# Kernel optimization log

Measured on AMD Instinct MI355X. Metric: run time of the kernel, lower is better.

Reference implementation:

```python
import jax, jax.numpy as jnp
import numpy as np

N = 100000      # nodes
E = 1600000     # edges (avg degree 16)
IN_DIM = 256
HID = 128
EPS = 0.3


def setup_inputs() -> dict:
    key = jax.random.key(0)
    ks = jax.random.split(key, 6)
    x = jax.random.normal(ks[0], (N, IN_DIM), dtype=jnp.float32)
    # edges without self-loops (dst = src + nonzero offset mod N)
    src = jax.random.randint(ks[1], (E,), 0, N)
    off = jax.random.randint(ks[2], (E,), 1, N)
    dst = (src + off) % N
    edge_index = jnp.stack([src, dst]).astype(jnp.int32)
    # xavier_normal_ with gain=1.414 for t1 and gate
    g1 = 1.414 * np.sqrt(2.0 / (IN_DIM + HID))
    w1 = (jax.random.normal(ks[3], (HID, IN_DIM)) * g1).astype(jnp.float32)
    b1 = jnp.zeros((HID,), jnp.float32)
    gg = 1.414 * np.sqrt(2.0 / (2 * HID + 1))
    gate_w = (jax.random.normal(ks[4], (1, 2 * HID)) * gg).astype(jnp.float32)
    gate_b = jnp.zeros((1,), jnp.float32)
    return dict(x=x, edge_index=edge_index, w1=w1, b1=b1, gate_w=gate_w, gate_b=gate_b)


def reference(x, edge_index, w1, b1, gate_w, gate_b):
    src, dst = edge_index[0], edge_index[1]
    # in-degree based symmetric norm, deg clamped to >= 1
    deg = jax.ops.segment_sum(jnp.ones((E,), jnp.float32), dst, num_segments=N)
    norm = jnp.clip(deg, 1.0) ** -0.5  # [N]

    h = jax.nn.relu(x @ w1.T + b1)     # [N, HID] (dropout p=0 / eval -> identity)
    raw = h

    # gate([h_dst, h_src]) decomposed: concat @ W^T = h_dst @ w_d + h_src @ w_s
    w_d, w_s = gate_w[0, :HID], gate_w[0, HID:]
    a_dst = h @ w_d                    # [N]
    a_src = h @ w_s                    # [N]
    g = jnp.tanh(a_dst[dst] + a_src[src] + gate_b[0])   # [E] per-edge gate
    e = g * norm[dst] * norm[src]                        # [E]

    # u_mul_e + sum: gather src features, weight, scatter-add to dst
    z = jax.ops.segment_sum(h[src] * e[:, None], dst, num_segments=N)  # [N, HID]
    return EPS * raw + z
```

## Files before the change

kernel.cpp:

```cpp
#include <hip/hip_runtime.h>
#include <math.h>
#include <stdint.h>

#define N_NODES 100000
#define N_EDGES 1600000
#define IN_DIM  256
#define HID     128
#define EPS_C   0.3f

#define NPB      128
#define NBKT     782
#define NBKT_P   784
#define BCAP     3072
#define S1_CHUNK 4096
#define S1_BLOCKS 391

#define PK_SRC(p)  ((p) & 0x1FFFF)
#define PK_LI(p)   ((p) >> 17)

typedef __attribute__((ext_vector_type(8))) __bf16 bf16x8;
typedef __attribute__((ext_vector_type(4))) float  f32x4;
typedef __attribute__((ext_vector_type(8))) unsigned short ushort8;

static __device__ __forceinline__ unsigned short f2bf(float f) {
    unsigned u = __float_as_uint(f);
    unsigned r = (u + 0x7fffu + ((u >> 16) & 1u)) >> 16;
    return (unsigned short)r;
}
static __device__ __forceinline__ float bf2f(unsigned short s) {
    return __uint_as_float((unsigned)s << 16);
}
static __device__ __forceinline__ float fast_tanh(float x) {
    float e = __builtin_exp2f(x * 2.8853900817779268f);
    return 1.0f - 2.0f / (e + 1.0f);
}

__global__ __launch_bounds__(256) void convert_w1_kernel(const float* __restrict__ w1,
                                                         unsigned short* __restrict__ w1b) {
    int i = blockIdx.x * 256 + threadIdx.x;
    if (i * 4 >= HID * IN_DIM) return;
    float4 v = *(const float4*)&w1[i * 4];
    ushort4 r;
    r.x = f2bf(v.x); r.y = f2bf(v.y); r.z = f2bf(v.z); r.w = f2bf(v.w);
    *(ushort4*)&w1b[i * 4] = r;
}

__global__ __launch_bounds__(512) void partition_kernel(const int* __restrict__ src,
                                                        const int* __restrict__ dst,
                                                        int* __restrict__ gcur,
                                                        int* __restrict__ ebuf) {
    __shared__ int hist[NBKT_P];
    __shared__ int base[NBKT_P];
    __shared__ int gpos[NBKT_P];
    __shared__ int cur[NBKT_P];
    __shared__ int seg[512];
    __shared__ int2 staged[S1_CHUNK];

    int t = threadIdx.x;
    for (int i = t; i < NBKT_P; i += 512) hist[i] = 0;
    __syncthreads();

    int base4 = blockIdx.x * (S1_CHUNK / 4);
    int rem4  = N_EDGES / 4 - base4;

    int4 sv[2], dv[2];
#pragma unroll
    for (int j = 0; j < 2; j++) {
        int i4 = j * 512 + t;
        if (i4 < rem4) {
            sv[j] = *(const int4*)&src[(base4 + i4) * 4];
            dv[j] = *(const int4*)&dst[(base4 + i4) * 4];
        } else {
            dv[j] = make_int4(-1, -1, -1, -1);
        }
    }
#pragma unroll
    for (int j = 0; j < 2; j++) {
        if (dv[j].x >= 0) {
            atomicAdd(&hist[dv[j].x >> 7], 1);
            atomicAdd(&hist[dv[j].y >> 7], 1);
            atomicAdd(&hist[dv[j].z >> 7], 1);
            atomicAdd(&hist[dv[j].w >> 7], 1);
        }
    }
    __syncthreads();

    int h0 = 0, h1 = 0;
    if (t < NBKT_P / 2) { h0 = hist[2 * t]; h1 = hist[2 * t + 1]; }
    seg[t] = h0 + h1;
    __syncthreads();
    for (int off = 1; off < 512; off <<= 1) {
        int a = (t >= off) ? seg[t - off] : 0;
        __syncthreads();
        seg[t] += a;
        __syncthreads();
    }
    if (t < NBKT_P / 2) {
        int excl = seg[t] - (h0 + h1);
        base[2 * t]     = excl;
        cur[2 * t]      = excl;
        base[2 * t + 1] = excl + h0;
        cur[2 * t + 1]  = excl + h0;
        if (h0 > 0) gpos[2 * t]     = atomicAdd(&gcur[2 * t], h0);
        if (h1 > 0) gpos[2 * t + 1] = atomicAdd(&gcur[2 * t + 1], h1);
    }
    __syncthreads();

#pragma unroll
    for (int j = 0; j < 2; j++) {
        if (dv[j].x >= 0) {
            int p;
            p = atomicAdd(&cur[dv[j].x >> 7], 1); staged[p] = make_int2(sv[j].x, dv[j].x);
            p = atomicAdd(&cur[dv[j].y >> 7], 1); staged[p] = make_int2(sv[j].y, dv[j].y);
            p = atomicAdd(&cur[dv[j].z >> 7], 1); staged[p] = make_int2(sv[j].z, dv[j].z);
            p = atomicAdd(&cur[dv[j].w >> 7], 1); staged[p] = make_int2(sv[j].w, dv[j].w);
        }
    }
    __syncthreads();

    int n = N_EDGES - base4 * 4;
    if (n > S1_CHUNK) n = S1_CHUNK;
    for (int i = t; i < n; i += 512) {
        int2 e = staged[i];
        int b = e.y >> 7;
        int off2 = gpos[b] + (i - base[b]);
        if (off2 < BCAP) ebuf[(size_t)b * BCAP + off2] = ((e.y & (NPB - 1)) << 17) | e.x;
    }
}

__global__ __launch_bounds__(512) void bscan_kernel(const int* __restrict__ gcur,
                                                    int* __restrict__ bstart) {
    __shared__ int s[512];
    int t = threadIdx.x;
    int a0 = 0, a1 = 0;
    if (t < NBKT_P / 2) {
        a0 = (2 * t     < NBKT) ? gcur[2 * t]     : 0;
        a1 = (2 * t + 1 < NBKT) ? gcur[2 * t + 1] : 0;
    }
    s[t] = a0 + a1;
    __syncthreads();
    for (int off = 1; off < 512; off <<= 1) {
        int a = (t >= off) ? s[t - off] : 0;
        __syncthreads();
        s[t] += a;
        __syncthreads();
    }
    if (t < NBKT_P / 2) {
        int excl = s[t] - (a0 + a1);
        if (2 * t     < NBKT) bstart[2 * t]     = excl;
        if (2 * t + 1 < NBKT) bstart[2 * t + 1] = excl + a0;
    }
}

__global__ __launch_bounds__(512) void deg_kernel(const int* __restrict__ gcur,
                                                  const int* __restrict__ bstart,
                                                  const int* __restrict__ ebuf,
                                                  int* __restrict__ rowstart,
                                                  float* __restrict__ nrm) {
    __shared__ int dcnt[NPB];
    __shared__ int s[NPB];
    int b = blockIdx.x;
    int t = threadIdx.x;
    if (t < NPB) dcnt[t] = 0;
    __syncthreads();

    int ecnt = gcur[b];
    if (ecnt > BCAP) ecnt = BCAP;
    for (int j = t; j < ecnt; j += 512)
        atomicAdd(&dcnt[PK_LI(ebuf[(size_t)b * BCAP + j])], 1);
    __syncthreads();

    int v = 0;
    if (t < NPB) { v = dcnt[t]; s[t] = v; }
    __syncthreads();
    for (int off = 1; off < NPB; off <<= 1) {
        int a = (t < NPB && t >= off) ? s[t - off] : 0;
        __syncthreads();
        if (t < NPB) s[t] += a;
        __syncthreads();
    }

    int nbase = b * NPB;
    int nn = N_NODES - nbase;
    if (nn > NPB) nn = NPB;
    if (t < nn) {
        rowstart[nbase + t] = bstart[b] + s[t] - v;
        nrm[nbase + t] = rsqrtf(fmaxf((float)v, 1.0f));
    }
    if (b == NBKT - 1 && t == 0) rowstart[N_NODES] = N_EDGES;
}

__global__ __launch_bounds__(256) void gemm_kernel(const float* __restrict__ x,
                                                   const unsigned short* __restrict__ w1b,
                                                   const float* __restrict__ b1,
                                                   const float* __restrict__ gw,
                                                   const float* __restrict__ nrm,
                                                   unsigned short* __restrict__ h,
                                                   float2* __restrict__ pd_pack,
                                                   float2* __restrict__ ps_pack) {
    __shared__ unsigned short As[256 * 40];
    __shared__ unsigned short Bs[128 * 40];

    int tid = threadIdx.x;
    int bm = blockIdx.x * 256;

    int wv   = tid >> 6;
    int lane = tid & 63;
    int col  = lane & 15;
    int kq   = lane >> 4;

    f32x4 acc[4][8];
#pragma unroll
    for (int f = 0; f < 4; f++)
#pragma unroll
        for (int nf = 0; nf < 8; nf++) acc[f][nf] = (f32x4){0.f, 0.f, 0.f, 0.f};

    int am = tid >> 2;
    int ak = (tid & 3) * 8;
    int bn = tid >> 1;
    int bk = (tid & 1) * 16;

    for (int k0 = 0; k0 < IN_DIM; k0 += 32) {
        ushort8 av[4];
#pragma unroll
        for (int sub = 0; sub < 4; sub++) {
            int r = am + sub * 64;
            float4 a0 = {0,0,0,0}, a1 = {0,0,0,0};
            if (bm + r < N_NODES) {
                const float* p = &x[(size_t)(bm + r) * IN_DIM + k0 + ak];
                a0 = *(const float4*)p;
                a1 = *(const float4*)(p + 4);
            }
            av[sub][0]=f2bf(a0.x); av[sub][1]=f2bf(a0.y);
            av[sub][2]=f2bf(a0.z); av[sub][3]=f2bf(a0.w);
            av[sub][4]=f2bf(a1.x); av[sub][5]=f2bf(a1.y);
            av[sub][6]=f2bf(a1.z); av[sub][7]=f2bf(a1.w);
        }
        ushort8 bv0 = *(const ushort8*)&w1b[bn * IN_DIM + k0 + bk];
        ushort8 bv1 = *(const ushort8*)&w1b[bn * IN_DIM + k0 + bk + 8];

        __syncthreads();
#pragma unroll
        for (int sub = 0; sub < 4; sub++)
            *(ushort8*)&As[(am + sub * 64) * 40 + ak] = av[sub];
        *(ushort8*)&Bs[bn * 40 + bk] = bv0;
        *(ushort8*)&Bs[bn * 40 + bk + 8] = bv1;
        __syncthreads();

        bf16x8 afrag[4];
#pragma unroll
        for (int f = 0; f < 4; f++)
            afrag[f] = *(bf16x8*)&As[(wv * 64 + f * 16 + col) * 40 + kq * 8];
#pragma unroll
        for (int nf = 0; nf < 8; nf++) {
            bf16x8 bfrag = *(bf16x8*)&Bs[(nf * 16 + col) * 40 + kq * 8];
#pragma unroll
            for (int f = 0; f < 4; f++)
                acc[f][nf] = __builtin_amdgcn_mfma_f32_16x16x32_bf16(afrag[f], bfrag,
                                                                     acc[f][nf], 0, 0, 0);
        }
    }

    float bias[8], wd[8], wsv[8];
#pragma unroll
    for (int nf = 0; nf < 8; nf++) {
        bias[nf] = b1[nf * 16 + col];
        wd[nf]   = gw[nf * 16 + col];
        wsv[nf]  = gw[HID + nf * 16 + col];
    }
#pragma unroll
    for (int f = 0; f < 4; f++) {
#pragma unroll
        for (int r = 0; r < 4; r++) {
            int gm = bm + wv * 64 + f * 16 + kq * 4 + r;
            float pd = 0.f, ps = 0.f;
            bool ok = (gm < N_NODES);
#pragma unroll
            for (int nf = 0; nf < 8; nf++) {
                float v = fmaxf(acc[f][nf][r] + bias[nf], 0.f);
                pd = fmaf(v, wd[nf], pd);
                ps = fmaf(v, wsv[nf], ps);
                if (ok) h[(size_t)gm * HID + nf * 16 + col] = f2bf(v);
            }
#pragma unroll
            for (int m = 1; m < 16; m <<= 1) {
                pd += __shfl_xor(pd, m);
                ps += __shfl_xor(ps, m);
            }
            if (ok && col == 0) {
                float nv = nrm[gm];
                pd_pack[gm] = make_float2(pd, nv);
                ps_pack[gm] = make_float2(ps, nv);
            }
        }
    }
}

__global__ __launch_bounds__(512) void scatter2_kernel(const int* __restrict__ gcur,
                                                       const int* __restrict__ ebuf,
                                                       const int* __restrict__ rowstart,
                                                       const float2* __restrict__ pd_pack,
                                                       const float2* __restrict__ ps_pack,
                                                       const float* __restrict__ gb,
                                                       int2* __restrict__ epack) {
    __shared__ int    curs[NPB];
    __shared__ float2 pdl[NPB];
    int b = blockIdx.x;
    int t = threadIdx.x;
    int nbase = b * NPB;
    int nn = N_NODES - nbase;
    if (nn > NPB) nn = NPB;
    if (t < nn) {
        curs[t] = rowstart[nbase + t];
        pdl[t]  = pd_pack[nbase + t];
    }
    __syncthreads();

    int ecnt = gcur[b];
    if (ecnt > BCAP) ecnt = BCAP;
    float gbv = gb[0];
    for (int j = t; j < ecnt; j += 512) {
        int p = ebuf[(size_t)b * BCAP + j];
        int s  = PK_SRC(p);
        int li = PK_LI(p);
        int pos = atomicAdd(&curs[li], 1);
        float2 pdp = pdl[li];
        float2 psp = ps_pack[s];
        float g = fast_tanh(pdp.x + psp.x + gbv);
        epack[pos] = make_int2(s, __float_as_int(g * pdp.y * psp.y));
    }
}

__global__ __launch_bounds__(256) void aggregate_kernel(const int* __restrict__ rowstart,
                                                        const int2* __restrict__ epack,
                                                        const unsigned short* __restrict__ h,
                                                        float* __restrict__ out) {
    int node = blockIdx.x * 4 + (threadIdx.x >> 6);
    if (node >= N_NODES) return;
    int lane = threadIdx.x & 63;
    int q  = lane >> 4;
    int ql = lane & 15;

    int beg = rowstart[node];
    int end = rowstart[node + 1];

    float acc[8];
#pragma unroll
    for (int t = 0; t < 8; t++) acc[t] = 0.f;

    int j = beg;
    for (; j + 8 <= end; j += 8) {
        int2 e0 = epack[j + q];
        int2 e1 = epack[j + 4 + q];
        ushort8 r0 = *(const ushort8*)&h[(size_t)e0.x * HID + ql * 8];
        ushort8 r1 = *(const ushort8*)&h[(size_t)e1.x * HID + ql * 8];
        float c0 = __int_as_float(e0.y);
        float c1 = __int_as_float(e1.y);
#pragma unroll
        for (int t = 0; t < 8; t++) {
            acc[t] = fmaf(c0, bf2f(r0[t]), acc[t]);
            acc[t] = fmaf(c1, bf2f(r1[t]), acc[t]);
        }
    }
    for (; j < end; j += 4) {
        bool act = (j + q) < end;
        int idx = act ? (j + q) : beg;
        int2 e = epack[idx];
        ushort8 r = *(const ushort8*)&h[(size_t)e.x * HID + ql * 8];
        float c = act ? __int_as_float(e.y) : 0.f;
#pragma unroll
        for (int t = 0; t < 8; t++) acc[t] = fmaf(c, bf2f(r[t]), acc[t]);
    }
#pragma unroll
    for (int t = 0; t < 8; t++) {
        acc[t] += __shfl_xor(acc[t], 16);
        acc[t] += __shfl_xor(acc[t], 32);
    }
    if (q == 0) {
        ushort8 hd = *(const ushort8*)&h[(size_t)node * HID + ql * 8];
        f32x4 o0, o1;
        o0.x = fmaf(EPS_C, bf2f(hd[0]), acc[0]);
        o0.y = fmaf(EPS_C, bf2f(hd[1]), acc[1]);
        o0.z = fmaf(EPS_C, bf2f(hd[2]), acc[2]);
        o0.w = fmaf(EPS_C, bf2f(hd[3]), acc[3]);
        o1.x = fmaf(EPS_C, bf2f(hd[4]), acc[4]);
        o1.y = fmaf(EPS_C, bf2f(hd[5]), acc[5]);
        o1.z = fmaf(EPS_C, bf2f(hd[6]), acc[6]);
        o1.w = fmaf(EPS_C, bf2f(hd[7]), acc[7]);
        __builtin_nontemporal_store(o0, (f32x4*)&out[(size_t)node * HID + ql * 8]);
        __builtin_nontemporal_store(o1, (f32x4*)&out[(size_t)node * HID + ql * 8 + 4]);
    }
}

extern "C" void kernel_launch(void* const* d_in, const int* in_sizes, int n_in,
                              void* d_out, int out_size, void* d_ws, size_t ws_size,
                              hipStream_t stream) {
    const float* x  = (const float*)d_in[0];
    const int*   ei = (const int*)d_in[1];
    const float* w1 = (const float*)d_in[2];
    const float* b1 = (const float*)d_in[3];
    const float* gw = (const float*)d_in[4];
    const float* gb = (const float*)d_in[5];
    float* out = (float*)d_out;

    const int* src = ei;
    const int* dst = ei + N_EDGES;

    uintptr_t base = (uintptr_t)d_ws;
    size_t off = 0;
    auto alloc = [&](size_t bytes) -> void* {
        void* p = (void*)(base + off);
        off += (bytes + 255) & ~(size_t)255;
        return p;
    };
    unsigned short* h   = (unsigned short*)alloc((size_t)N_NODES * HID * 2);
    float2* pd_pack     = (float2*)alloc((size_t)N_NODES * 8);
    float2* ps_pack     = (float2*)alloc((size_t)N_NODES * 8);
    float*  nrm         = (float*)alloc((size_t)N_NODES * 4);
    int*    rowstart    = (int*)alloc((size_t)(N_NODES + 1) * 4);
    int2*   epack       = (int2*)alloc((size_t)N_EDGES * 8);
    unsigned short* w1b = (unsigned short*)alloc((size_t)HID * IN_DIM * 2);
    int*    gcur        = (int*)alloc((size_t)NBKT * 4);
    int*    bstart      = (int*)alloc((size_t)NBKT * 4);
    int*    ebuf        = (int*)alloc((size_t)NBKT * BCAP * 4);

    (void)hipMemsetAsync(gcur, 0, (size_t)NBKT * 4, stream);

    convert_w1_kernel<<<(HID * IN_DIM / 4 + 255) / 256, 256, 0, stream>>>(w1, w1b);
    partition_kernel<<<S1_BLOCKS, 512, 0, stream>>>(src, dst, gcur, ebuf);
    bscan_kernel<<<1, 512, 0, stream>>>(gcur, bstart);
    deg_kernel<<<NBKT, 512, 0, stream>>>(gcur, bstart, ebuf, rowstart, nrm);
    gemm_kernel<<<(N_NODES + 255) / 256, 256, 0, stream>>>(x, w1b, b1, gw, nrm,
                                                           h, pd_pack, ps_pack);
    scatter2_kernel<<<NBKT, 512, 0, stream>>>(gcur, ebuf, rowstart,
                                              pd_pack, ps_pack, gb, epack);
    aggregate_kernel<<<(N_NODES + 3) / 4, 256, 0, stream>>>(rowstart, epack, h, out);
}
```

Baseline: 313.9 us.

## Simplify edge partition, drop bucket scan, restructure GEMM with resident swizzled W

The partition kernel now writes packed edges straight to global buckets from LDS atomic cursors instead of staging and locally scanning them. Bucket counters are padded to 16 ints each to avoid contention on shared cache lines. The global bucket scan kernel is removed: each bucket owns a fixed BCAP-sized region of epack, and per-node (begin, end) pairs are stored as int2. The GEMM is rewritten to keep all of W1 in swizzled LDS, use 128-row tiles with one 16-row MFMA strip per wave, and prefetch A in registers, dropping per-k LDS staging and barriers. The trade-off is scattered global writes in partition and a larger, padded edge buffer.

```diff
diff --git a/kernel.cpp b/kernel.cpp
--- a/kernel.cpp
+++ b/kernel.cpp
@@ -14,6 +14,7 @@
 #define BCAP     3072
 #define S1_CHUNK 4096
 #define S1_BLOCKS 391
+#define GC(b)    ((b) * 16)
 
 #define PK_SRC(p)  ((p) & 0x1FFFF)
 #define PK_LI(p)   ((p) >> 17)
@@ -50,11 +51,7 @@
                                                         int* __restrict__ gcur,
                                                         int* __restrict__ ebuf) {
     __shared__ int hist[NBKT_P];
-    __shared__ int base[NBKT_P];
-    __shared__ int gpos[NBKT_P];
     __shared__ int cur[NBKT_P];
-    __shared__ int seg[512];
-    __shared__ int2 staged[S1_CHUNK];
 
     int t = threadIdx.x;
     for (int i = t; i < NBKT_P; i += 512) hist[i] = 0;
@@ -85,77 +82,32 @@
     }
     __syncthreads();
 
-    int h0 = 0, h1 = 0;
-    if (t < NBKT_P / 2) { h0 = hist[2 * t]; h1 = hist[2 * t + 1]; }
-    seg[t] = h0 + h1;
-    __syncthreads();
-    for (int off = 1; off < 512; off <<= 1) {
-        int a = (t >= off) ? seg[t - off] : 0;
-        __syncthreads();
-        seg[t] += a;
-        __syncthreads();
-    }
     if (t < NBKT_P / 2) {
-        int excl = seg[t] - (h0 + h1);
-        base[2 * t]     = excl;
-        cur[2 * t]      = excl;
-        base[2 * t + 1] = excl + h0;
-        cur[2 * t + 1]  = excl + h0;
-        if (h0 > 0) gpos[2 * t]     = atomicAdd(&gcur[2 * t], h0);
-        if (h1 > 0) gpos[2 * t + 1] = atomicAdd(&gcur[2 * t + 1], h1);
+        int h0 = hist[2 * t], h1 = hist[2 * t + 1];
+        if (h0 > 0) cur[2 * t]     = atomicAdd(&gcur[GC(2 * t)], h0);
+        if (h1 > 0) cur[2 * t + 1] = atomicAdd(&gcur[GC(2 * t + 1)], h1);
     }
     __syncthreads();
 
 #pragma unroll
     for (int j = 0; j < 2; j++) {
         if (dv[j].x >= 0) {
-            int p;
-            p = atomicAdd(&cur[dv[j].x >> 7], 1); staged[p] = make_int2(sv[j].x, dv[j].x);
-            p = atomicAdd(&cur[dv[j].y >> 7], 1); staged[p] = make_int2(sv[j].y, dv[j].y);
-            p = atomicAdd(&cur[dv[j].z >> 7], 1); staged[p] = make_int2(sv[j].z, dv[j].z);
-            p = atomicAdd(&cur[dv[j].w >> 7], 1); staged[p] = make_int2(sv[j].w, dv[j].w);
-        }
-    }
-    __syncthreads();
-
-    int n = N_EDGES - base4 * 4;
-    if (n > S1_CHUNK) n = S1_CHUNK;
-    for (int i = t; i < n; i += 512) {
-        int2 e = staged[i];
-        int b = e.y >> 7;
-        int off2 = gpos[b] + (i - base[b]);
-        if (off2 < BCAP) ebuf[(size_t)b * BCAP + off2] = ((e.y & (NPB - 1)) << 17) | e.x;
-    }
-}
-
-__global__ __launch_bounds__(512) void bscan_kernel(const int* __restrict__ gcur,
-                                                    int* __restrict__ bstart) {
-    __shared__ int s[512];
-    int t = threadIdx.x;
-    int a0 = 0, a1 = 0;
-    if (t < NBKT_P / 2) {
-        a0 = (2 * t     < NBKT) ? gcur[2 * t]     : 0;
-        a1 = (2 * t + 1 < NBKT) ? gcur[2 * t + 1] : 0;
-    }
-    s[t] = a0 + a1;
-    __syncthreads();
-    for (int off = 1; off < 512; off <<= 1) {
-        int a = (t >= off) ? s[t - off] : 0;
-        __syncthreads();
-        s[t] += a;
-        __syncthreads();
-    }
-    if (t < NBKT_P / 2) {
-        int excl = s[t] - (a0 + a1);
-        if (2 * t     < NBKT) bstart[2 * t]     = excl;
-        if (2 * t + 1 < NBKT) bstart[2 * t + 1] = excl + a0;
+            int b, p;
+            b = dv[j].x >> 7; p = atomicAdd(&cur[b], 1);
+            if (p < BCAP) ebuf[(size_t)b * BCAP + p] = ((dv[j].x & (NPB - 1)) << 17) | sv[j].x;
+            b = dv[j].y >> 7; p = atomicAdd(&cur[b], 1);
+            if (p < BCAP) ebuf[(size_t)b * BCAP + p] = ((dv[j].y & (NPB - 1)) << 17) | sv[j].y;
+            b = dv[j].z >> 7; p = atomicAdd(&cur[b], 1);
+            if (p < BCAP) ebuf[(size_t)b * BCAP + p] = ((dv[j].z & (NPB - 1)) << 17) | sv[j].z;
+            b = dv[j].w >> 7; p = atomicAdd(&cur[b], 1);
+            if (p < BCAP) ebuf[(size_t)b * BCAP + p] = ((dv[j].w & (NPB - 1)) << 17) | sv[j].w;
+        }
     }
 }
 
 __global__ __launch_bounds__(512) void deg_kernel(const int* __restrict__ gcur,
-                                                  const int* __restrict__ bstart,
                                                   const int* __restrict__ ebuf,
-                                                  int* __restrict__ rowstart,
+                                                  int2* __restrict__ rs2,
                                                   float* __restrict__ nrm) {
     __shared__ int dcnt[NPB];
     __shared__ int s[NPB];
@@ -164,7 +116,7 @@
     if (t < NPB) dcnt[t] = 0;
     __syncthreads();
 
-    int ecnt = gcur[b];
+    int ecnt = gcur[GC(b)];
     if (ecnt > BCAP) ecnt = BCAP;
     for (int j = t; j < ecnt; j += 512)
         atomicAdd(&dcnt[PK_LI(ebuf[(size_t)b * BCAP + j])], 1);
@@ -184,13 +136,13 @@
     int nn = N_NODES - nbase;
     if (nn > NPB) nn = NPB;
     if (t < nn) {
-        rowstart[nbase + t] = bstart[b] + s[t] - v;
+        int incl = s[t];
+        rs2[nbase + t] = make_int2(b * BCAP + incl - v, b * BCAP + incl);
         nrm[nbase + t] = rsqrtf(fmaxf((float)v, 1.0f));
     }
-    if (b == NBKT - 1 && t == 0) rowstart[N_NODES] = N_EDGES;
-}
-
-__global__ __launch_bounds__(256) void gemm_kernel(const float* __restrict__ x,
+}
+
+__global__ __launch_bounds__(512) void gemm_kernel(const float* __restrict__ x,
                                                    const unsigned short* __restrict__ w1b,
                                                    const float* __restrict__ b1,
                                                    const float* __restrict__ gw,
@@ -198,67 +150,58 @@
                                                    unsigned short* __restrict__ h,
                                                    float2* __restrict__ pd_pack,
                                                    float2* __restrict__ ps_pack) {
-    __shared__ unsigned short As[256 * 40];
-    __shared__ unsigned short Bs[128 * 40];
-
-    int tid = threadIdx.x;
-    int bm = blockIdx.x * 256;
-
+    __shared__ unsigned short Bs[HID * IN_DIM];
+
+    int tid  = threadIdx.x;
+    int bm   = blockIdx.x * 128;
     int wv   = tid >> 6;
     int lane = tid & 63;
     int col  = lane & 15;
     int kq   = lane >> 4;
 
-    f32x4 acc[4][8];
-#pragma unroll
-    for (int f = 0; f < 4; f++)
-#pragma unroll
-        for (int nf = 0; nf < 8; nf++) acc[f][nf] = (f32x4){0.f, 0.f, 0.f, 0.f};
-
-    int am = tid >> 2;
-    int ak = (tid & 3) * 8;
-    int bn = tid >> 1;
-    int bk = (tid & 1) * 16;
+    {
+        int n   = tid >> 2;
+        int k8b = (tid & 3) * 8;
+        const ushort8* srcp = (const ushort8*)&w1b[n * IN_DIM + k8b * 8];
+#pragma unroll
+        for (int j = 0; j < 8; j++) {
+            int k8 = k8b + j;
+            *(ushort8*)((char*)Bs + n * 512 + ((k8 ^ (n & 7)) * 16)) = srcp[j];
+        }
+    }
+
+    f32x4 acc[8];
+#pragma unroll
+    for (int nf = 0; nf < 8; nf++) acc[nf] = (f32x4){0.f, 0.f, 0.f, 0.f};
+
+    int row  = bm + wv * 16 + col;
+    bool rok = row < N_NODES;
+    const float* ap = &x[(size_t)row * IN_DIM + kq * 8];
+
+    float4 a0 = {0, 0, 0, 0}, a1 = {0, 0, 0, 0};
+    if (rok) { a0 = *(const float4*)ap; a1 = *(const float4*)(ap + 4); }
+
+    __syncthreads();
 
     for (int k0 = 0; k0 < IN_DIM; k0 += 32) {
-        ushort8 av[4];
-#pragma unroll
-        for (int sub = 0; sub < 4; sub++) {
-            int r = am + sub * 64;
-            float4 a0 = {0,0,0,0}, a1 = {0,0,0,0};
-            if (bm + r < N_NODES) {
-                const float* p = &x[(size_t)(bm + r) * IN_DIM + k0 + ak];
-                a0 = *(const float4*)p;
-                a1 = *(const float4*)(p + 4);
-            }
-            av[sub][0]=f2bf(a0.x); av[sub][1]=f2bf(a0.y);
-            av[sub][2]=f2bf(a0.z); av[sub][3]=f2bf(a0.w);
-            av[sub][4]=f2bf(a1.x); av[sub][5]=f2bf(a1.y);
-            av[sub][6]=f2bf(a1.z); av[sub][7]=f2bf(a1.w);
-        }
-        ushort8 bv0 = *(const ushort8*)&w1b[bn * IN_DIM + k0 + bk];
-        ushort8 bv1 = *(const ushort8*)&w1b[bn * IN_DIM + k0 + bk + 8];
-
-        __syncthreads();
-#pragma unroll
-        for (int sub = 0; sub < 4; sub++)
-            *(ushort8*)&As[(am + sub * 64) * 40 + ak] = av[sub];
-        *(ushort8*)&Bs[bn * 40 + bk] = bv0;
-        *(ushort8*)&Bs[bn * 40 + bk + 8] = bv1;
-        __syncthreads();
-
-        bf16x8 afrag[4];
-#pragma unroll
-        for (int f = 0; f < 4; f++)
-            afrag[f] = *(bf16x8*)&As[(wv * 64 + f * 16 + col) * 40 + kq * 8];
+        float4 n0 = {0, 0, 0, 0}, n1 = {0, 0, 0, 0};
+        if (k0 + 32 < IN_DIM && rok) {
+            n0 = *(const float4*)(ap + k0 + 32);
+            n1 = *(const float4*)(ap + k0 + 36);
+        }
+        ushort8 av;
+        av[0] = f2bf(a0.x); av[1] = f2bf(a0.y); av[2] = f2bf(a0.z); av[3] = f2bf(a0.w);
+        av[4] = f2bf(a1.x); av[5] = f2bf(a1.y); av[6] = f2bf(a1.z); av[7] = f2bf(a1.w);
+        bf16x8 afrag = *(bf16x8*)&av;
+
+        int swz = ((k0 >> 3) + kq) ^ (col & 7);
 #pragma unroll
         for (int nf = 0; nf < 8; nf++) {
-            bf16x8 bfrag = *(bf16x8*)&Bs[(nf * 16 + col) * 40 + kq * 8];
-#pragma unroll
-            for (int f = 0; f < 4; f++)
-                acc[f][nf] = __builtin_amdgcn_mfma_f32_16x16x32_bf16(afrag[f], bfrag,
-                                                                     acc[f][nf], 0, 0, 0);
-        }
+            int n = nf * 16 + col;
+            bf16x8 bfrag = *(bf16x8*)((char*)Bs + n * 512 + swz * 16);
+            acc[nf] = __builtin_amdgcn_mfma_f32_16x16x32_bf16(afrag, bfrag, acc[nf], 0, 0, 0);
+        }
+        a0 = n0; a1 = n1;
     }
 
     float bias[8], wd[8], wsv[8];
@@ -269,36 +212,33 @@
         wsv[nf]  = gw[HID + nf * 16 + col];
     }
 #pragma unroll
-    for (int f = 0; f < 4; f++) {
-#pragma unroll
-        for (int r = 0; r < 4; r++) {
-            int gm = bm + wv * 64 + f * 16 + kq * 4 + r;
-            float pd = 0.f, ps = 0.f;
-            bool ok = (gm < N_NODES);
-#pragma unroll
-            for (int nf = 0; nf < 8; nf++) {
-                float v = fmaxf(acc[f][nf][r] + bias[nf], 0.f);
-                pd = fmaf(v, wd[nf], pd);
-                ps = fmaf(v, wsv[nf], ps);
-                if (ok) h[(size_t)gm * HID + nf * 16 + col] = f2bf(v);
-            }
-#pragma unroll
-            for (int m = 1; m < 16; m <<= 1) {
-                pd += __shfl_xor(pd, m);
-                ps += __shfl_xor(ps, m);
-            }
-            if (ok && col == 0) {
-                float nv = nrm[gm];
-                pd_pack[gm] = make_float2(pd, nv);
-                ps_pack[gm] = make_float2(ps, nv);
-            }
+    for (int r = 0; r < 4; r++) {
+        int gm = bm + wv * 16 + kq * 4 + r;
+        float pd = 0.f, ps = 0.f;
+        bool ok = (gm < N_NODES);
+#pragma unroll
+        for (int nf = 0; nf < 8; nf++) {
+            float v = fmaxf(acc[nf][r] + bias[nf], 0.f);
+            pd = fmaf(v, wd[nf], pd);
+            ps = fmaf(v, wsv[nf], ps);
+            if (ok) h[(size_t)gm * HID + nf * 16 + col] = f2bf(v);
+        }
+#pragma unroll
+        for (int m = 1; m < 16; m <<= 1) {
+            pd += __shfl_xor(pd, m);
+            ps += __shfl_xor(ps, m);
+        }
+        if (ok && col == 0) {
+            float nv = nrm[gm];
+            pd_pack[gm] = make_float2(pd, nv);
+            ps_pack[gm] = make_float2(ps, nv);
         }
     }
 }
 
 __global__ __launch_bounds__(512) void scatter2_kernel(const int* __restrict__ gcur,
                                                        const int* __restrict__ ebuf,
-                                                       const int* __restrict__ rowstart,
+                                                       const int2* __restrict__ rs2,
                                                        const float2* __restrict__ pd_pack,
                                                        const float2* __restrict__ ps_pack,
                                                        const float* __restrict__ gb,
@@ -311,12 +251,12 @@
     int nn = N_NODES - nbase;
     if (nn > NPB) nn = NPB;
     if (t < nn) {
-        curs[t] = rowstart[nbase + t];
+        curs[t] = rs2[nbase + t].x;
         pdl[t]  = pd_pack[nbase + t];
     }
     __syncthreads();
 
-    int ecnt = gcur[b];
+    int ecnt = gcur[GC(b)];
     if (ecnt > BCAP) ecnt = BCAP;
     float gbv = gb[0];
     for (int j = t; j < ecnt; j += 512) {
@@ -331,7 +271,7 @@
     }
 }
 
-__global__ __launch_bounds__(256) void aggregate_kernel(const int* __restrict__ rowstart,
+__global__ __launch_bounds__(256) void aggregate_kernel(const int2* __restrict__ rs2,
                                                         const int2* __restrict__ epack,
                                                         const unsigned short* __restrict__ h,
                                                         float* __restrict__ out) {
@@ -341,8 +281,9 @@
     int q  = lane >> 4;
     int ql = lane & 15;
 
-    int beg = rowstart[node];
-    int end = rowstart[node + 1];
+    int2 be = rs2[node];
+    int beg = be.x;
+    int end = be.y;
 
     float acc[8];
 #pragma unroll
@@ -417,22 +358,20 @@
     float2* pd_pack     = (float2*)alloc((size_t)N_NODES * 8);
     float2* ps_pack     = (float2*)alloc((size_t)N_NODES * 8);
     float*  nrm         = (float*)alloc((size_t)N_NODES * 4);
-    int*    rowstart    = (int*)alloc((size_t)(N_NODES + 1) * 4);
-    int2*   epack       = (int2*)alloc((size_t)N_EDGES * 8);
+    int2*   rs2         = (int2*)alloc((size_t)N_NODES * 8);
+    int2*   epack       = (int2*)alloc((size_t)NBKT * BCAP * 8);
     unsigned short* w1b = (unsigned short*)alloc((size_t)HID * IN_DIM * 2);
-    int*    gcur        = (int*)alloc((size_t)NBKT * 4);
-    int*    bstart      = (int*)alloc((size_t)NBKT * 4);
+    int*    gcur        = (int*)alloc((size_t)NBKT * 16 * 4);
     int*    ebuf        = (int*)alloc((size_t)NBKT * BCAP * 4);
 
-    (void)hipMemsetAsync(gcur, 0, (size_t)NBKT * 4, stream);
+    (void)hipMemsetAsync(gcur, 0, (size_t)NBKT * 16 * 4, stream);
 
     convert_w1_kernel<<<(HID * IN_DIM / 4 + 255) / 256, 256, 0, stream>>>(w1, w1b);
     partition_kernel<<<S1_BLOCKS, 512, 0, stream>>>(src, dst, gcur, ebuf);
-    bscan_kernel<<<1, 512, 0, stream>>>(gcur, bstart);
-    deg_kernel<<<NBKT, 512, 0, stream>>>(gcur, bstart, ebuf, rowstart, nrm);
-    gemm_kernel<<<(N_NODES + 255) / 256, 256, 0, stream>>>(x, w1b, b1, gw, nrm,
+    deg_kernel<<<NBKT, 512, 0, stream>>>(gcur, ebuf, rs2, nrm);
+    gemm_kernel<<<(N_NODES + 127) / 128, 512, 0, stream>>>(x, w1b, b1, gw, nrm,
                                                            h, pd_pack, ps_pack);
-    scatter2_kernel<<<NBKT, 512, 0, stream>>>(gcur, ebuf, rowstart,
+    scatter2_kernel<<<NBKT, 512, 0, stream>>>(gcur, ebuf, rs2,
                                               pd_pack, ps_pack, gb, epack);
-    aggregate_kernel<<<(N_NODES + 3) / 4, 256, 0, stream>>>(rowstart, epack, h, out);
-}
+    aggregate_kernel<<<(N_NODES + 3) / 4, 256, 0, stream>>>(rs2, epack, h, out);
+}
```

After: 306.0 us. 1.03x faster.
